# Kernel optimization log

Measured on AMD Instinct MI355X. Metric: run time of the kernel, lower is better.

The kernel has to match this reference:

```python
import jax, jax.numpy as jnp
import numpy as np

N_DRUG, N_DIS = 3072, 3072
N = N_DRUG + N_DIS
E = 196608
F1, F2, F3 = 512, 256, 128
GAMMA1 = GAMMA2 = GAMMA3 = 0.03125
NEG_SLOPE = 0.2   # GATConv default negative_slope
KERNEL_W = 0.25   # drug_ps/dis_ps = 1/kernel_len


def gat_layer(x, src, dst, w_e, W, a_src, a_dst, b):
    """Single-head GATConv: gather -> per-node softmax -> scatter-aggregate.
    Edge weights w_e scale the unnormalized attention."""
    xw = x @ W                                                  # [N, F]
    e = jax.nn.leaky_relu((xw @ a_src)[src] + (xw @ a_dst)[dst], NEG_SLOPE)  # [E]
    m = jax.ops.segment_max(e, dst, num_segments=N)
    ex = jnp.exp(e - m[dst]) * w_e
    denom = jax.ops.segment_sum(ex, dst, num_segments=N)
    alpha = ex / (denom[dst] + 1e-16)
    out = jax.ops.segment_sum(alpha[:, None] * xw[src], dst, num_segments=N)
    return out + b


def gip_kernel(y, gamma):
    """getGipKernel(y, 0, gamma, normalized=True)."""
    mn = jnp.min(y, axis=1, keepdims=True)
    mx = jnp.max(y, axis=1, keepdims=True)
    y = (y - mn) / (mx - mn + 1e-12)          # row-wise min-max normalize
    k = y @ y.T
    k = k / jnp.mean(jnp.diagonal(k))
    d = jnp.diagonal(k)
    dist = d[:, None] + d[None, :] - 2.0 * k  # kernelToDistance
    return jnp.exp(-gamma * dist)


def normalized_kernel(K):
    K = jnp.abs(K)
    minv = jnp.min(jnp.where(K > 0, K, jnp.inf))
    K = jnp.where(K == 0, minv, K)            # replace zeros with min nonzero
    d = jnp.sqrt(jnp.diagonal(K))
    return K / (d[:, None] * d[None, :])


def setup_inputs() -> dict:
    key = jax.random.key(0)
    ks = jax.random.split(key, 20)
    f32 = jnp.float32

    def lin(k, fi, fo):
        return jax.random.normal(k, (fi, fo), f32) * (1.0 / float(np.sqrt(fi)))

    inp = {
        'x': jax.random.normal(ks[0], (N, N), f32),
        'edge_index': jax.random.randint(ks[1], (2, E), 0, N, dtype=jnp.int32),
        'adj_data': jax.random.uniform(ks[2], (N, N), f32),
        'drug_sim': jax.random.uniform(ks[3], (N_DRUG, N_DRUG), f32),
        'dis_sim': jax.random.uniform(ks[4], (N_DIS, N_DIS), f32),
        'alpha1': jax.random.normal(ks[5], (N_DRUG, N_DIS), f32),
        'alpha2': jax.random.normal(ks[6], (N_DIS, N_DRUG), f32),
        'W1': lin(ks[7], N, F1),
        'as1': jax.random.normal(ks[8], (F1,), f32) * 0.1,
        'ad1': jax.random.normal(ks[9], (F1,), f32) * 0.1,
        'b1': jnp.zeros((F1,), f32),
        'W2': lin(ks[10], F1, F2),
        'as2': jax.random.normal(ks[11], (F2,), f32) * 0.1,
        'ad2': jax.random.normal(ks[12], (F2,), f32) * 0.1,
        'b2': jnp.zeros((F2,), f32),
        'W3': lin(ks[13], F2, F3),
        'as3': jax.random.normal(ks[14], (F3,), f32) * 0.1,
        'ad3': jax.random.normal(ks[15], (F3,), f32) * 0.1,
        'b3': jnp.zeros((F3,), f32),
    }
    return inp


def reference(x, edge_index, adj_data, drug_sim, dis_sim, alpha1, alpha2,
              W1, as1, ad1, b1, W2, as2, ad2, b2, W3, as3, ad3, b3):
    src0, dst0 = edge_index[0], edge_index[1]
    w0 = adj_data[src0, dst0]                  # per-edge gather of dense weights
    loop = jnp.arange(N, dtype=src0.dtype)     # GATConv add_self_loops=True
    src = jnp.concatenate([src0, loop])
    dst = jnp.concatenate([dst0, loop])
    w = jnp.concatenate([w0, jnp.ones((N,), adj_data.dtype)])

    H1 = jax.nn.relu(gat_layer(x, src, dst, w, W1, as1, ad1, b1))
    H2 = jax.nn.relu(gat_layer(H1, src, dst, w, W2, as2, ad2, b2))
    H3 = jax.nn.relu(gat_layer(H2, src, dst, w, W3, as3, ad3, b3))

    drug_k = KERNEL_W * (gip_kernel(H1[:N_DRUG], GAMMA1)
                         + gip_kernel(H2[:N_DRUG], GAMMA2)
                         + gip_kernel(H3[:N_DRUG], GAMMA3) + drug_sim)
    dis_k = KERNEL_W * (gip_kernel(H1[N_DRUG:], GAMMA1)
                        + gip_kernel(H2[N_DRUG:], GAMMA2)
                        + gip_kernel(H3[N_DRUG:], GAMMA3) + dis_sim)

    out1 = normalized_kernel(drug_k) @ alpha1  # [N_DRUG, N_DIS]
    out2 = normalized_kernel(dis_k) @ alpha2   # [N_DIS, N_DRUG]
    return 0.5 * (out1 + out2.T)
```

## Files before the change

kernel.cpp:

```cpp
#include <hip/hip_runtime.h>
#include <hip/hip_bf16.h>
#include <stdint.h>

#define N_NODES 6144
#define N_DRUG  3072
#define N_EDGE  196608
#define E_TOT   (N_EDGE + N_NODES)
#define GAMMA   0.03125f

typedef __bf16 bf16x8 __attribute__((ext_vector_type(8)));
typedef float  f32x4  __attribute__((ext_vector_type(4)));

__device__ __forceinline__ unsigned short f2b(float f){
  union { float f; unsigned u; } v; v.f = f;
  unsigned r = v.u + 0x7FFFu + ((v.u >> 16) & 1u);
  return (unsigned short)(r >> 16);
}
__device__ __forceinline__ float b2f(unsigned short b){
  union { unsigned u; float f; } v; v.u = ((unsigned)b) << 16;
  return v.f;
}
__device__ __forceinline__ void gl_lds(const void* g, void* l){
  __builtin_amdgcn_global_load_lds((const __attribute__((address_space(1))) void*)g,
                                   (__attribute__((address_space(3))) void*)l, 16, 0, 0);
}

#define WAITVM(N) asm volatile("s_waitcnt vmcnt(" #N ")" ::: "memory")
#define SYNC() { __builtin_amdgcn_sched_barrier(0); __builtin_amdgcn_s_barrier(); __builtin_amdgcn_sched_barrier(0); }

__global__ void cast_bf16_k(const float* __restrict__ in, unsigned short* __restrict__ out, long n){
  long i = ((long)blockIdx.x*blockDim.x + threadIdx.x)*4;
  long stride = (long)gridDim.x*blockDim.x*4;
  for (; i < n; i += stride){
    float4 v = *(const float4*)(in + i);
    ushort4 o;
    o.x = f2b(v.x); o.y = f2b(v.y); o.z = f2b(v.z); o.w = f2b(v.w);
    *(ushort4*)(out + i) = o;
  }
}

__global__ void tcast_k(const float* __restrict__ in, unsigned short* __restrict__ out,
                        int R, int Cd, int OLD, int OOFF){
  __shared__ float tile[32][33];
  int bx = blockIdx.x*32, by = blockIdx.y*32;
  int tx = threadIdx.x, ty = threadIdx.y;
  for (int i = ty; i < 32; i += 8) tile[i][tx] = in[(long)(by+i)*Cd + bx + tx];
  __syncthreads();
  for (int i = ty; i < 32; i += 8) out[(long)(bx+i)*OLD + OOFF + by + tx] = f2b(tile[tx][i]);
}

__global__ void hist_k(const int* __restrict__ ei, int* __restrict__ cnt){
  int i = blockIdx.x*blockDim.x + threadIdx.x;
  if (i >= E_TOT) return;
  int d = (i < N_EDGE) ? ei[N_EDGE + i] : (i - N_EDGE);
  atomicAdd(&cnt[d], 1);
}

__global__ void scan_k(const int* __restrict__ cnt, int* __restrict__ ptr){
  __shared__ int sums[1024];
  int t = threadIdx.x;
  int v[6]; int s = 0;
  #pragma unroll
  for (int i = 0; i < 6; i++){ v[i] = s; s += cnt[t*6 + i]; }
  sums[t] = s; __syncthreads();
  for (int off = 1; off < 1024; off <<= 1){
    int add = (t >= off) ? sums[t - off] : 0;
    __syncthreads();
    sums[t] += add;
    __syncthreads();
  }
  int base = (t == 0) ? 0 : sums[t-1];
  #pragma unroll
  for (int i = 0; i < 6; i++) ptr[t*6 + i] = base + v[i];
  if (t == 1023) ptr[N_NODES] = sums[1023];
}

__global__ void scatter_k(const int* __restrict__ ei, const int* __restrict__ ptr,
                          int* __restrict__ cur, int* __restrict__ srcs,
                          int* __restrict__ epos){
  int i = blockIdx.x*blockDim.x + threadIdx.x;
  if (i >= E_TOT) return;
  int s = (i < N_EDGE) ? ei[i] : (i - N_EDGE);
  int d = (i < N_EDGE) ? ei[N_EDGE + i] : (i - N_EDGE);
  int pos = ptr[d] + atomicAdd(&cur[d], 1);
  srcs[pos] = s; epos[i] = pos;
}

__global__ void dots_k(const float* __restrict__ XW, const float* __restrict__ av,
                       const float* __restrict__ dv, float* __restrict__ es,
                       float* __restrict__ ed, float* __restrict__ denom, int F){
  int n = blockIdx.x, l = threadIdx.x;
  float s = 0.f, d = 0.f;
  for (int f = l; f < F; f += 64){
    float x = XW[(long)n*F + f];
    s += x * av[f]; d += x * dv[f];
  }
  #pragma unroll
  for (int off = 32; off > 0; off >>= 1){ s += __shfl_down(s, off); d += __shfl_down(d, off); }
  if (l == 0){ es[n] = s; ed[n] = d; denom[n] = 0.f; }
}

__global__ void phase12_k(const int* __restrict__ ei, const float* __restrict__ adj,
                          const float* __restrict__ es, const float* __restrict__ ed,
                          const int* __restrict__ epos, float* __restrict__ exc,
                          float* __restrict__ denom){
  int i = blockIdx.x*blockDim.x + threadIdx.x;
  if (i >= E_TOT) return;
  int s = (i < N_EDGE) ? ei[i] : (i - N_EDGE);
  int d = (i < N_EDGE) ? ei[N_EDGE + i] : (i - N_EDGE);
  float w = (i < N_EDGE) ? adj[(long)s*N_NODES + d] : 1.0f;
  float e = es[s] + ed[d];
  e = (e > 0.f) ? e : 0.2f*e;
  float ex = expf(e) * w;
  exc[epos[i]] = ex;
  atomicAdd(&denom[d], ex);
}

__global__ void agg4_k(const float* __restrict__ XW, const int* __restrict__ ptr,
                       const int* __restrict__ srcs, const float* __restrict__ exc,
                       const float* __restrict__ denom, const float* __restrict__ bias,
                       float* __restrict__ H, unsigned short* __restrict__ Hb, int F){
  int n = blockIdx.x, t = threadIdx.x;
  int st = ptr[n], en = ptr[n+1];
  float a0v = 0.f, a1v = 0.f, a2v = 0.f, a3v = 0.f;
  int j = st;
  for (; j + 1 < en; j += 2){
    float w0 = exc[j], w1 = exc[j+1];
    int s0 = srcs[j], s1 = srcs[j+1];
    float4 v0 = *(const float4*)(XW + (long)s0*F + t*4);
    float4 v1 = *(const float4*)(XW + (long)s1*F + t*4);
    a0v += w0*v0.x + w1*v1.x; a1v += w0*v0.y + w1*v1.y;
    a2v += w0*v0.z + w1*v1.z; a3v += w0*v0.w + w1*v1.w;
  }
  if (j < en){
    float w0 = exc[j]; int s0 = srcs[j];
    float4 v0 = *(const float4*)(XW + (long)s0*F + t*4);
    a0v += w0*v0.x; a1v += w0*v0.y; a2v += w0*v0.z; a3v += w0*v0.w;
  }
  float invd = 1.f/(denom[n] + 1e-16f);
  float4 b = *(const float4*)(bias + t*4);
  float4 o;
  o.x = fmaxf(a0v*invd + b.x, 0.f); o.y = fmaxf(a1v*invd + b.y, 0.f);
  o.z = fmaxf(a2v*invd + b.z, 0.f); o.w = fmaxf(a3v*invd + b.w, 0.f);
  *(float4*)(H + (long)n*F + t*4) = o;
  if (Hb){
    ushort4 ob; ob.x = f2b(o.x); ob.y = f2b(o.y); ob.z = f2b(o.z); ob.w = f2b(o.w);
    *(ushort4*)(Hb + (long)n*F + t*4) = ob;
  }
}

__global__ void agg_k(const float* __restrict__ XW, const int* __restrict__ ptr,
                      const int* __restrict__ srcs, const float* __restrict__ exc,
                      const float* __restrict__ denom, const float* __restrict__ bias,
                      float* __restrict__ H, unsigned short* __restrict__ Hb, int F){
  int n = blockIdx.x, t = threadIdx.x;
  int st = ptr[n], en = ptr[n+1];
  float ax = 0.f, ay = 0.f;
  int j = st;
  for (; j + 1 < en; j += 2){
    float a0 = exc[j], a1 = exc[j+1];
    int s0 = srcs[j], s1 = srcs[j+1];
    float2 v0 = *(const float2*)(XW + (long)s0*F + t*2);
    float2 v1 = *(const float2*)(XW + (long)s1*F + t*2);
    ax += a0*v0.x + a1*v1.x;
    ay += a0*v0.y + a1*v1.y;
  }
  if (j < en){
    float a = exc[j];
    int s = srcs[j];
    float2 v = *(const float2*)(XW + (long)s*F + t*2);
    ax += a*v.x; ay += a*v.y;
  }
  float invd = 1.f/(denom[n] + 1e-16f);
  float2 b = *(const float2*)(bias + t*2);
  float vx = fmaxf(ax*invd + b.x, 0.f);
  float vy = fmaxf(ay*invd + b.y, 0.f);
  *(float2*)(H + (long)n*F + t*2) = make_float2(vx, vy);
  if (Hb){
    ushort2 o; o.x = f2b(vx); o.y = f2b(vy);
    *(ushort2*)(Hb + (long)n*F + t*2) = o;
  }
}

__global__ void rownorm_all_k(const float* __restrict__ H0, const float* __restrict__ H1,
                              const float* __restrict__ H2,
                              unsigned short* __restrict__ y0, unsigned short* __restrict__ y1,
                              float* __restrict__ dv0, float* __restrict__ dv1){
  int seg = blockIdx.y;
  int side = seg / 3, layer = seg % 3;
  int F = 512 >> layer;
  const float* H = (layer == 0) ? H0 : (layer == 1) ? H1 : H2;
  H += (size_t)(side ? N_DRUG : 0) * F;
  unsigned short* yb = ((side ? y1 : y0) + ((layer == 0) ? 0 : (layer == 1) ? 512 : 768));
  float* dvec = (side ? dv1 : dv0) + layer*N_DRUG;

  int r = blockIdx.x, t = threadIdx.x;
  __shared__ float ra[256], rb[256];
  float mn = 3.4e38f, mx = -3.4e38f;
  for (int f = t; f < F; f += 256){
    float v = H[(long)r*F + f];
    mn = fminf(mn, v); mx = fmaxf(mx, v);
  }
  ra[t] = mn; rb[t] = mx; __syncthreads();
  for (int s2 = 128; s2 > 0; s2 >>= 1){
    if (t < s2){ ra[t] = fminf(ra[t], ra[t+s2]); rb[t] = fmaxf(rb[t], rb[t+s2]); }
    __syncthreads();
  }
  mn = ra[0]; mx = rb[0];
  __syncthreads();
  float sc = 1.f/(mx - mn + 1e-12f);
  float s = 0.f;
  for (int f = t; f < F; f += 256){
    float v = (H[(long)r*F + f] - mn)*sc;
    unsigned short b = f2b(v);
    yb[(long)r*896 + f] = b;
    float vb = b2f(b);
    s += vb*vb;
  }
  ra[t] = s; __syncthreads();
  for (int s2 = 128; s2 > 0; s2 >>= 1){
    if (t < s2) ra[t] += ra[t+s2];
    __syncthreads();
  }
  if (t == 0) dvec[r] = ra[0];
}

__global__ void vecsum_all_k(const float* __restrict__ dv0, const float* __restrict__ dv1,
                             float* __restrict__ sump){
  int seg = blockIdx.y;
  int side = seg / 3, layer = seg % 3;
  const float* v = (side ? dv1 : dv0) + layer*N_DRUG;
  __shared__ float red[256];
  int t = threadIdx.x;
  float s = 0.f;
  for (int i = blockIdx.x*256 + t; i < N_DRUG; i += gridDim.x*256) s += v[i];
  red[t] = s; __syncthreads();
  for (int s2 = 128; s2 > 0; s2 >>= 1){ if (t < s2) red[t] += red[t+s2]; __syncthreads(); }
  if (t == 0) atomicAdd(&sump[seg], red[0]);
}

__global__ void diag3_all_k(const float* __restrict__ sim0, const float* __restrict__ sim1,
                            float* __restrict__ rs0, float* __restrict__ rs1){
  int i = blockIdx.x*256 + threadIdx.x;
  const float* sim = blockIdx.y ? sim1 : sim0;
  float* rs = blockIdx.y ? rs1 : rs0;
  if (i < N_DRUG) rs[i] = rsqrtf(sim[(long)i*N_DRUG + i] + 3.0f);
}

template<int EPI>
__global__ __launch_bounds__(512, 2) void gemm8p(
    const unsigned short* __restrict__ A, const unsigned short* __restrict__ Bt,
    float* __restrict__ P, int M, int N, int K, int kz)
{
  __shared__ unsigned short lds[2][2][16384];
  int t = threadIdx.x;
  int lane = t & 63, wave = t >> 6;
  int wm = wave >> 2, wn = wave & 3;

  int nbx = gridDim.x;
  int nwg = nbx * gridDim.y;
  int bid = blockIdx.y * nbx + blockIdx.x;
  int cpx = nwg >> 3;
  int swz = (bid & 7) * cpx + (bid >> 3);
  long brow = (long)(swz / nbx) * 256;
  long bcol = (long)(swz % nbx) * 256;
  long k0 = (long)blockIdx.z * kz;
  int nt = kz >> 6;

  int sr = wave*8 + (lane >> 3);
  int cg = (lane & 7) ^ (lane >> 3);
  const unsigned short* gA = A  + (brow + sr)*(long)K + k0 + cg*8;
  const unsigned short* gB = Bt + (bcol + sr)*(long)K + k0 + cg*8;
  unsigned ldsw = wave * 512;

  auto stage = [&](int b, int mat, int h, int tk){
    const unsigned short* g = (mat ? gB : gA) + (long)(h*128)*K + (long)tk*64;
    unsigned short* d = &lds[b][mat][h*8192 + ldsw];
    gl_lds(g, d);
    gl_lds(g + (long)64*K, d + 4096);
  };

  int fr = lane & 15, q = lane >> 4;
  int lo = fr*64 + ((q ^ (fr & 7))*8);
  int dk = (lo ^ 32) - lo;

  f32x4 acc[8][4];
  #pragma unroll
  for (int a = 0; a < 8; a++)
    #pragma unroll
    for (int b = 0; b < 4; b++){ acc[a][b][0]=0.f; acc[a][b][1]=0.f; acc[a][b][2]=0.f; acc[a][b][3]=0.f; }
  bf16x8 af[4][2], bf[4][2];

  const unsigned short* a0p = &lds[0][0][wm*8192 + lo];
  const unsigned short* b0p = &lds[0][1][wn*4096 + lo];
  const unsigned short* a1p = &lds[1][0][wm*8192 + lo];
  const unsigned short* b1p = &lds[1][1][wn*4096 + lo];

#define RD_AF_LO(ab) { _Pragma("unroll") for (int j = 0; j < 4; ++j){ \
    af[j][0] = *(const bf16x8*)((ab) + j*1024); af[j][1] = *(const bf16x8*)((ab) + j*1024 + dk); } }
#define RD_AF_HI(ab) { _Pragma("unroll") for (int j = 0; j < 4; ++j){ \
    af[j][0] = *(const bf16x8*)((ab) + (4+j)*1024); af[j][1] = *(const bf16x8*)((ab) + (4+j)*1024 + dk); } }
#define RD_BF_LO(bb) { _Pragma("unroll") for (int j = 0; j < 2; ++j){ \
    bf[j][0] = *(const bf16x8*)((bb) + j*1024); bf[j][1] = *(const bf16x8*)((bb) + j*1024 + dk); } }
#define RD_BF_HI(bb) { _Pragma("unroll") for (int j = 2; j < 4; ++j){ \
    bf[j][0] = *(const bf16x8*)((bb) + j*1024); bf[j][1] = *(const bf16x8*)((bb) + j*1024 + dk); } }
#define MFMA_Q(MB, NB) { __builtin_amdgcn_s_setprio(1); \
    _Pragma("unroll") for (int mi = 0; mi < 4; ++mi) \
      _Pragma("unroll") for (int ni = (NB); ni < (NB)+2; ++ni) \
        _Pragma("unroll") for (int kk = 0; kk < 2; ++kk) \
          acc[(MB)+mi][ni] = __builtin_amdgcn_mfma_f32_16x16x32_bf16(af[mi][kk], bf[ni][kk], acc[(MB)+mi][ni], 0, 0, 0); \
    __builtin_amdgcn_s_setprio(0); }

  stage(0,0,0,0); stage(0,0,1,0); stage(0,1,0,0); stage(0,1,1,0);
  stage(1,1,0,1); stage(1,1,1,1);
  WAITVM(4);
  SYNC();

  int half = nt >> 1;
  for (int i = 0; i < half; ++i){
    int t1 = 2*i+1, t2 = 2*i+2, t3 = 2*i+3;
    bool s2 = t2 < nt, s3 = t3 < nt;
    RD_AF_LO(a0p); RD_BF_LO(b0p);
    stage(1,0,0,t1);
    SYNC(); MFMA_Q(0,0); SYNC();
    RD_BF_HI(b0p);
    stage(1,0,1,t1);
    SYNC(); MFMA_Q(0,2); SYNC();
    RD_AF_HI(a0p);
    if (s2) stage(0,1,0,t2);
    SYNC(); MFMA_Q(4,0); SYNC();
    if (s2){ stage(0,1,1,t2); WAITVM(4); } else { WAITVM(0); }
    SYNC(); MFMA_Q(4,2); SYNC();
    RD_AF_LO(a1p); RD_BF_LO(b1p);
    if (s2) stage(0,0,0,t2);
    SYNC(); MFMA_Q(0,0); SYNC();
    RD_BF_HI(b1p);
    if (s2) stage(0,0,1,t2);
    SYNC(); MFMA_Q(0,2); SYNC();
    RD_AF_HI(a1p);
    if (s3) stage(1,1,0,t3);
    SYNC(); MFMA_Q(4,0); SYNC();
    if (s3){ stage(1,1,1,t3); WAITVM(4); } else { WAITVM(0); }
    SYNC(); MFMA_Q(4,2); SYNC();
  }
#undef RD_AF_LO
#undef RD_AF_HI
#undef RD_BF_LO
#undef RD_BF_HI
#undef MFMA_Q

  float* Pz = P + (long)blockIdx.z*M*N;
  #pragma unroll
  for (int mi = 0; mi < 8; ++mi){
    #pragma unroll
    for (int ni = 0; ni < 4; ++ni){
      long col = bcol + wn*64 + ni*16 + fr;
      #pragma unroll
      for (int r = 0; r < 4; ++r){
        long row = brow + wm*128 + mi*16 + q*4 + r;
        float v = acc[mi][ni][r];
        if (EPI == 0) Pz[row*N + col] = v;
        else          Pz[row*N + col] = 0.5f*v;
      }
    }
  }
}

__global__ void reduce4_k(const float* __restrict__ p, float* __restrict__ out, long n){
  long i = ((long)blockIdx.x*blockDim.x + threadIdx.x)*4;
  if (i >= n) return;
  float4 s = *(const float4*)(p + i);
  #pragma unroll
  for (int z = 1; z < 4; z++){
    float4 x = *(const float4*)(p + (long)z*n + i);
    s.x += x.x; s.y += x.y; s.z += x.z; s.w += x.w;
  }
  *(float4*)(out + i) = s;
}

template<int EPI>
__global__ __launch_bounds__(256) void gemm_tn(
    const unsigned short* __restrict__ A, const unsigned short* __restrict__ Bt,
    float* __restrict__ C, int M, int N, int K)
{
  __shared__ unsigned short As[2][128*64];
  __shared__ unsigned short Bs[2][128*64];
  int t = threadIdx.x;
  int wave = t >> 6, lane = t & 63;
  int brow = blockIdx.y*128, bcol = blockIdx.x*128;
  int wr = (wave >> 1)*64, wc = (wave & 1)*64;
  int fr = lane & 15, q = lane >> 4;
  int rin = lane >> 3, kslot = (lane & 7) ^ rin;

  f32x4 acc[4][4];
  #pragma unroll
  for (int a = 0; a < 4; a++)
    #pragma unroll
    for (int b = 0; b < 4; b++){ acc[a][b][0]=0.f; acc[a][b][1]=0.f; acc[a][b][2]=0.f; acc[a][b][3]=0.f; }

  int aoff[4][2], boff[4][2];
  #pragma unroll
  for (int mi = 0; mi < 4; mi++){
    int row = wr + mi*16 + fr;
    #pragma unroll
    for (int kk = 0; kk < 2; kk++) aoff[mi][kk] = row*64 + (((kk*4 + q) ^ (row & 7))*8);
  }
  #pragma unroll
  for (int ni = 0; ni < 4; ni++){
    int row = wc + ni*16 + fr;
    #pragma unroll
    for (int kk = 0; kk < 2; kk++) boff[ni][kk] = row*64 + (((kk*4 + q) ^ (row & 7))*8);
  }

  auto stage = [&](int buf, int k0){
    #pragma unroll
    for (int p = 0; p < 4; p++){
      int rsec = p*32 + wave*8;
      gl_lds(A  + (long)(brow + rsec + rin)*K + k0 + kslot*8, &As[buf][rsec*64]);
      gl_lds(Bt + (long)(bcol + rsec + rin)*K + k0 + kslot*8, &Bs[buf][rsec*64]);
    }
  };

  int nsteps = K >> 6;
  stage(0, 0);
  __syncthreads();
  int curb = 0;
  for (int s = 0; s < nsteps; s++){
    if (s + 1 < nsteps) stage(curb ^ 1, (s + 1)*64);
    const unsigned short* a_l = As[curb];
    const unsigned short* b_l = Bs[curb];
    #pragma unroll
    for (int kk = 0; kk < 2; kk++){
      bf16x8 af[4], bfv[4];
      #pragma unroll
      for (int mi = 0; mi < 4; mi++) af[mi]  = *(const bf16x8*)(a_l + aoff[mi][kk]);
      #pragma unroll
      for (int ni = 0; ni < 4; ni++) bfv[ni] = *(const bf16x8*)(b_l + boff[ni][kk]);
      #pragma unroll
      for (int mi = 0; mi < 4; mi++)
        #pragma unroll
        for (int ni = 0; ni < 4; ni++)
          acc[mi][ni] = __builtin_amdgcn_mfma_f32_16x16x32_bf16(af[mi], bfv[ni], acc[mi][ni], 0, 0, 0);
    }
    __syncthreads();
    curb ^= 1;
  }

  #pragma unroll
  for (int mi = 0; mi < 4; mi++){
    #pragma unroll
    for (int ni = 0; ni < 4; ni++){
      int col = bcol + wc + ni*16 + fr;
      #pragma unroll
      for (int r = 0; r < 4; r++){
        int row = brow + wr + mi*16 + q*4 + r;
        long idx = (long)row*N + col;
        float v = acc[mi][ni][r];
        if (EPI == 0) C[idx] = v;
        else          C[idx] = 0.5f*v;
      }
    }
  }
}

__global__ __launch_bounds__(512) void gip_gemm(
    const unsigned short* __restrict__ Y, const float* __restrict__ sim,
    const float* __restrict__ dv, const float* __restrict__ sums,
    const float* __restrict__ rs, unsigned short* __restrict__ outp, int outoff)
{
  __shared__ unsigned short As[2][128*64];
  __shared__ unsigned short Bs[2][128*64];
  const int K = 896;
  int t = threadIdx.x;
  int wave = t >> 6, lane = t & 63;
  int brow = blockIdx.y*128, bcol = blockIdx.x*128;
  int wr = (wave >> 1)*32, wc = (wave & 1)*64;
  int fr = lane & 15, q = lane >> 4;
  int rin = lane >> 3, kslot = (lane & 7) ^ rin;

  f32x4 acc0[2][4], acc1[2][4], acc2[2][4];
  #pragma unroll
  for (int a = 0; a < 2; a++)
    #pragma unroll
    for (int b = 0; b < 4; b++){
      acc0[a][b][0]=0.f;acc0[a][b][1]=0.f;acc0[a][b][2]=0.f;acc0[a][b][3]=0.f;
      acc1[a][b][0]=0.f;acc1[a][b][1]=0.f;acc1[a][b][2]=0.f;acc1[a][b][3]=0.f;
      acc2[a][b][0]=0.f;acc2[a][b][1]=0.f;acc2[a][b][2]=0.f;acc2[a][b][3]=0.f;
    }

  int aoff[2][2], boff[4][2];
  #pragma unroll
  for (int mi = 0; mi < 2; mi++){
    int row = wr + mi*16 + fr;
    #pragma unroll
    for (int kk = 0; kk < 2; kk++) aoff[mi][kk] = row*64 + (((kk*4 + q) ^ (row & 7))*8);
  }
  #pragma unroll
  for (int ni = 0; ni < 4; ni++){
    int row = wc + ni*16 + fr;
    #pragma unroll
    for (int kk = 0; kk < 2; kk++) boff[ni][kk] = row*64 + (((kk*4 + q) ^ (row & 7))*8);
  }

  auto stage = [&](int buf, int k0){
    #pragma unroll
    for (int p = 0; p < 2; p++){
      int rsec = p*64 + wave*8;
      gl_lds(Y + (long)(brow + rsec + rin)*K + k0 + kslot*8, &As[buf][rsec*64]);
      gl_lds(Y + (long)(bcol + rsec + rin)*K + k0 + kslot*8, &Bs[buf][rsec*64]);
    }
  };

  int curb = 0, s = 0;
  stage(0, 0);
  __syncthreads();

#define GSTEP(ACC) { \
    if (s + 1 < 14) stage(curb ^ 1, (s + 1)*64); \
    const unsigned short* a_l = As[curb]; \
    const unsigned short* b_l = Bs[curb]; \
    _Pragma("unroll") \
    for (int kk = 0; kk < 2; kk++){ \
      bf16x8 af0 = *(const bf16x8*)(a_l + aoff[0][kk]); \
      bf16x8 af1 = *(const bf16x8*)(a_l + aoff[1][kk]); \
      _Pragma("unroll") \
      for (int ni = 0; ni < 4; ni++){ \
        bf16x8 bv = *(const bf16x8*)(b_l + boff[ni][kk]); \
        ACC[0][ni] = __builtin_amdgcn_mfma_f32_16x16x32_bf16(af0, bv, ACC[0][ni], 0, 0, 0); \
        ACC[1][ni] = __builtin_amdgcn_mfma_f32_16x16x32_bf16(af1, bv, ACC[1][ni], 0, 0, 0); \
      } \
    } \
    __syncthreads(); curb ^= 1; s++; }

  for (int i = 0; i < 8; i++) GSTEP(acc0)
  for (int i = 0; i < 4; i++) GSTEP(acc1)
  for (int i = 0; i < 2; i++) GSTEP(acc2)
#undef GSTEP

  float im0 = (float)N_DRUG / sums[0];
  float im1 = (float)N_DRUG / sums[1];
  float im2 = (float)N_DRUG / sums[2];
  #pragma unroll
  for (int mi = 0; mi < 2; mi++){
    #pragma unroll
    for (int ni = 0; ni < 4; ni++){
      int col = bcol + wc + ni*16 + fr;
      float d0c = dv[col], d1c = dv[N_DRUG + col], d2c = dv[2*N_DRUG + col];
      float rc = rs[col];
      #pragma unroll
      for (int r = 0; r < 4; r++){
        int row = brow + wr + mi*16 + q*4 + r;
        float v = sim[(long)row*N_DRUG + col]
                + expf(-GAMMA*((dv[row]            + d0c - 2.f*acc0[mi][ni][r])*im0))
                + expf(-GAMMA*((dv[N_DRUG + row]   + d1c - 2.f*acc1[mi][ni][r])*im1))
                + expf(-GAMMA*((dv[2*N_DRUG + row] + d2c - 2.f*acc2[mi][ni][r])*im2));
        outp[(long)row*N_NODES + outoff + col] = f2b(v * rs[row] * rc);
      }
    }
  }
}

extern "C" void kernel_launch(void* const* d_in, const int* in_sizes, int n_in,
                              void* d_out, int out_size, void* d_ws, size_t ws_size,
                              hipStream_t stream){
  const float* x        = (const float*)d_in[0];
  const int*   ei       = (const int*)d_in[1];
  const float* adj      = (const float*)d_in[2];
  const float* drug_sim = (const float*)d_in[3];
  const float* dis_sim  = (const float*)d_in[4];
  const float* alpha1   = (const float*)d_in[5];
  const float* alpha2   = (const float*)d_in[6];
  const float* W[3]   = {(const float*)d_in[7],  (const float*)d_in[11], (const float*)d_in[15]};
  const float* as_[3] = {(const float*)d_in[8],  (const float*)d_in[12], (const float*)d_in[16]};
  const float* ad_[3] = {(const float*)d_in[9],  (const float*)d_in[13], (const float*)d_in[17]};
  const float* bs_[3] = {(const float*)d_in[10], (const float*)d_in[14], (const float*)d_in[18]};
  float* out = (float*)d_out;
  const int Fs[3] = {512, 256, 128};

  char* p = (char*)d_ws;
  auto alloc = [&](size_t bytes)->char*{
    char* r = p; p += (bytes + 255) & ~(size_t)255; return r;
  };
  unsigned short* xb  = (unsigned short*)alloc((size_t)N_NODES*N_NODES*2);
  unsigned short* wb  = (unsigned short*)alloc((size_t)N_NODES*512*2);
  float* XW           = (float*)alloc((size_t)N_NODES*512*4);
  float* Hf[3];
  Hf[0] = (float*)alloc((size_t)N_NODES*512*4);
  Hf[1] = (float*)alloc((size_t)N_NODES*256*4);
  Hf[2] = (float*)alloc((size_t)N_NODES*128*4);
  unsigned short* Hb  = (unsigned short*)alloc((size_t)N_NODES*512*2);
  float* es    = (float*)alloc(N_NODES*4);
  float* edv   = (float*)alloc(N_NODES*4);
  float* denom = (float*)alloc(N_NODES*4);
  float* exc   = (float*)alloc((size_t)E_TOT*4);
  int* cntcur  = (int*)alloc((size_t)2*N_NODES*4);
  int* cnt = cntcur, *cur = cntcur + N_NODES;
  int* cptr = (int*)alloc((N_NODES+1)*4);
  int* srcs = (int*)alloc((size_t)E_TOT*4);
  int* epos = (int*)alloc((size_t)E_TOT*4);
  unsigned short* ycat[2];
  ycat[0] = (unsigned short*)alloc((size_t)N_DRUG*896*2);
  ycat[1] = (unsigned short*)alloc((size_t)N_DRUG*896*2);
  float* dvv[2];
  dvv[0] = (float*)alloc((size_t)3*N_DRUG*4);
  dvv[1] = (float*)alloc((size_t)3*N_DRUG*4);
  float* sump = (float*)alloc(256);
  float* rsv[2];
  rsv[0] = (float*)alloc(N_DRUG*4);
  rsv[1] = (float*)alloc(N_DRUG*4);
  unsigned short* Abuf  = (unsigned short*)alloc((size_t)N_DRUG*N_NODES*2);
  unsigned short* Btbuf = (unsigned short*)alloc((size_t)N_DRUG*N_NODES*2);

  float* pL1 = (float*)Abuf;

  cast_bf16_k<<<4096, 256, 0, stream>>>(x, xb, (long)N_NODES*N_NODES);
  hipMemsetAsync(cntcur, 0, (size_t)2*N_NODES*4, stream);
  hist_k<<<(E_TOT+255)/256, 256, 0, stream>>>(ei, cnt);
  scan_k<<<1, 1024, 0, stream>>>(cnt, cptr);
  scatter_k<<<(E_TOT+255)/256, 256, 0, stream>>>(ei, cptr, cur, srcs, epos);

  const unsigned short* Ain = xb;
  int Kin = N_NODES;
  for (int l = 0; l < 3; l++){
    int F = Fs[l];
    tcast_k<<<dim3(F/32, Kin/32), dim3(32,8), 0, stream>>>(W[l], wb, Kin, F, Kin, 0);
    if (l == 0){
      gemm8p<0><<<dim3(F/256, N_NODES/256, 4), 512, 0, stream>>>(Ain, wb, pL1, N_NODES, F, Kin, Kin/4);
      reduce4_k<<<(int)(((long)N_NODES*F/4 + 255)/256), 256, 0, stream>>>(pL1, XW, (long)N_NODES*F);
    } else {
      gemm_tn<0><<<dim3(F/128, N_NODES/128), 256, 0, stream>>>(Ain, wb, XW, N_NODES, F, Kin);
    }
    dots_k<<<N_NODES, 64, 0, stream>>>(XW, as_[l], ad_[l], es, edv, denom, F);
    phase12_k<<<(E_TOT+255)/256, 256, 0, stream>>>(ei, adj, es, edv, epos, exc, denom);
    unsigned short* HbOut = (l < 2) ? Hb : nullptr;
    if (F >= 256)
      agg4_k<<<N_NODES, F/4, 0, stream>>>(XW, cptr, srcs, exc, denom, bs_[l], Hf[l], HbOut, F);
    else
      agg_k<<<N_NODES, F/2, 0, stream>>>(XW, cptr, srcs, exc, denom, bs_[l], Hf[l], HbOut, F);
    Ain = Hb; Kin = F;
  }

  hipMemsetAsync(sump, 0, 24, stream);
  rownorm_all_k<<<dim3(N_DRUG, 6), 256, 0, stream>>>(Hf[0], Hf[1], Hf[2],
                                                     ycat[0], ycat[1], dvv[0], dvv[1]);
  vecsum_all_k<<<dim3(12, 6), 256, 0, stream>>>(dvv[0], dvv[1], sump);
  diag3_all_k<<<dim3(N_DRUG/256, 2), 256, 0, stream>>>(drug_sim, dis_sim, rsv[0], rsv[1]);

  tcast_k<<<dim3(N_DRUG/32, N_DRUG/32), dim3(32,8), 0, stream>>>(alpha2, Abuf,  N_DRUG, N_DRUG, N_NODES, N_DRUG);
  tcast_k<<<dim3(N_DRUG/32, N_DRUG/32), dim3(32,8), 0, stream>>>(alpha1, Btbuf, N_DRUG, N_DRUG, N_NODES, 0);

  gip_gemm<<<dim3(N_DRUG/128, N_DRUG/128), 512, 0, stream>>>(ycat[0], drug_sim, dvv[0], sump,     rsv[0], Abuf, 0);
  gip_gemm<<<dim3(N_DRUG/128, N_DRUG/128), 512, 0, stream>>>(ycat[1], dis_sim,  dvv[1], sump + 3, rsv[1], Btbuf, N_DRUG);

  gemm8p<2><<<dim3(N_DRUG/256, N_DRUG/256, 1), 512, 0, stream>>>(Abuf, Btbuf, out, N_DRUG, N_DRUG, N_NODES, N_NODES);

  (void)in_sizes; (void)n_in; (void)out_size; (void)ws_size;
}
```

Baseline: 671.8 us.

## Split-K final GEMM, bf16 aggregation gathers, and merge small kernel launches

The final 3072x3072x6144 GEMM is split three ways along K, launching three times as many blocks. The three fp32 partials are then summed and halved in a separate reduce kernel. The GEMMs that produce XW now also write a bf16 copy, so the edge aggregation gathers half the bytes per neighbour. The per-row diagonal sum is folded into rownorm with atomics, and the paired tcast and gip_gemm launches are merged into single launches using a z grid dimension. The costs are extra partial-buffer traffic, bf16 rounding in the aggregation inputs, and reuse of the xb and XW workspace areas as scratch for the partials.

Result: slower. 816.8 us (+21.6%).

```diff
diff --git a/kernel.cpp b/kernel.cpp
--- a/kernel.cpp
+++ b/kernel.cpp
@@ -47,6 +47,19 @@
   for (int i = ty; i < 32; i += 8) tile[i][tx] = in[(long)(by+i)*Cd + bx + tx];
   __syncthreads();
   for (int i = ty; i < 32; i += 8) out[(long)(bx+i)*OLD + OOFF + by + tx] = f2b(tile[tx][i]);
+}
+
+__global__ void tcast2_k(const float* __restrict__ a2, const float* __restrict__ a1,
+                         unsigned short* __restrict__ o0, unsigned short* __restrict__ o1){
+  __shared__ float tile[32][33];
+  const float* in = blockIdx.z ? a1 : a2;
+  unsigned short* out = blockIdx.z ? o1 : o0;
+  int OOFF = blockIdx.z ? 0 : N_DRUG;
+  int bx = blockIdx.x*32, by = blockIdx.y*32;
+  int tx = threadIdx.x, ty = threadIdx.y;
+  for (int i = ty; i < 32; i += 8) tile[i][tx] = in[(long)(by+i)*N_DRUG + bx + tx];
+  __syncthreads();
+  for (int i = ty; i < 32; i += 8) out[(long)(bx+i)*N_NODES + OOFF + by + tx] = f2b(tile[tx][i]);
 }
 
 __global__ void hist_k(const int* __restrict__ ei, int* __restrict__ cnt){
@@ -116,7 +129,7 @@
   atomicAdd(&denom[d], ex);
 }
 
-__global__ void agg4_k(const float* __restrict__ XW, const int* __restrict__ ptr,
+__global__ void agg4_k(const unsigned short* __restrict__ XWb, const int* __restrict__ ptr,
                        const int* __restrict__ srcs, const float* __restrict__ exc,
                        const float* __restrict__ denom, const float* __restrict__ bias,
                        float* __restrict__ H, unsigned short* __restrict__ Hb, int F){
@@ -127,15 +140,15 @@
   for (; j + 1 < en; j += 2){
     float w0 = exc[j], w1 = exc[j+1];
     int s0 = srcs[j], s1 = srcs[j+1];
-    float4 v0 = *(const float4*)(XW + (long)s0*F + t*4);
-    float4 v1 = *(const float4*)(XW + (long)s1*F + t*4);
-    a0v += w0*v0.x + w1*v1.x; a1v += w0*v0.y + w1*v1.y;
-    a2v += w0*v0.z + w1*v1.z; a3v += w0*v0.w + w1*v1.w;
+    ushort4 u0 = *(const ushort4*)(XWb + (long)s0*F + t*4);
+    ushort4 u1 = *(const ushort4*)(XWb + (long)s1*F + t*4);
+    a0v += w0*b2f(u0.x) + w1*b2f(u1.x); a1v += w0*b2f(u0.y) + w1*b2f(u1.y);
+    a2v += w0*b2f(u0.z) + w1*b2f(u1.z); a3v += w0*b2f(u0.w) + w1*b2f(u1.w);
   }
   if (j < en){
     float w0 = exc[j]; int s0 = srcs[j];
-    float4 v0 = *(const float4*)(XW + (long)s0*F + t*4);
-    a0v += w0*v0.x; a1v += w0*v0.y; a2v += w0*v0.z; a3v += w0*v0.w;
+    ushort4 u0 = *(const ushort4*)(XWb + (long)s0*F + t*4);
+    a0v += w0*b2f(u0.x); a1v += w0*b2f(u0.y); a2v += w0*b2f(u0.z); a3v += w0*b2f(u0.w);
   }
   float invd = 1.f/(denom[n] + 1e-16f);
   float4 b = *(const float4*)(bias + t*4);
@@ -149,7 +162,7 @@
   }
 }
 
-__global__ void agg_k(const float* __restrict__ XW, const int* __restrict__ ptr,
+__global__ void agg_k(const unsigned short* __restrict__ XWb, const int* __restrict__ ptr,
                       const int* __restrict__ srcs, const float* __restrict__ exc,
                       const float* __restrict__ denom, const float* __restrict__ bias,
                       float* __restrict__ H, unsigned short* __restrict__ Hb, int F){
@@ -160,16 +173,15 @@
   for (; j + 1 < en; j += 2){
     float a0 = exc[j], a1 = exc[j+1];
     int s0 = srcs[j], s1 = srcs[j+1];
-    float2 v0 = *(const float2*)(XW + (long)s0*F + t*2);
-    float2 v1 = *(const float2*)(XW + (long)s1*F + t*2);
-    ax += a0*v0.x + a1*v1.x;
-    ay += a0*v0.y + a1*v1.y;
+    ushort2 u0 = *(const ushort2*)(XWb + (long)s0*F + t*2);
+    ushort2 u1 = *(const ushort2*)(XWb + (long)s1*F + t*2);
+    ax += a0*b2f(u0.x) + a1*b2f(u1.x);
+    ay += a0*b2f(u0.y) + a1*b2f(u1.y);
   }
   if (j < en){
-    float a = exc[j];
-    int s = srcs[j];
-    float2 v = *(const float2*)(XW + (long)s*F + t*2);
-    ax += a*v.x; ay += a*v.y;
+    float a = exc[j]; int s = srcs[j];
+    ushort2 u = *(const ushort2*)(XWb + (long)s*F + t*2);
+    ax += a*b2f(u.x); ay += a*b2f(u.y);
   }
   float invd = 1.f/(denom[n] + 1e-16f);
   float2 b = *(const float2*)(bias + t*2);
@@ -185,7 +197,8 @@
 __global__ void rownorm_all_k(const float* __restrict__ H0, const float* __restrict__ H1,
                               const float* __restrict__ H2,
                               unsigned short* __restrict__ y0, unsigned short* __restrict__ y1,
-                              float* __restrict__ dv0, float* __restrict__ dv1){
+                              float* __restrict__ dv0, float* __restrict__ dv1,
+                              float* __restrict__ sump){
   int seg = blockIdx.y;
   int side = seg / 3, layer = seg % 3;
   int F = 512 >> layer;
@@ -222,21 +235,7 @@
     if (t < s2) ra[t] += ra[t+s2];
     __syncthreads();
   }
-  if (t == 0) dvec[r] = ra[0];
-}
-
-__global__ void vecsum_all_k(const float* __restrict__ dv0, const float* __restrict__ dv1,
-                             float* __restrict__ sump){
-  int seg = blockIdx.y;
-  int side = seg / 3, layer = seg % 3;
-  const float* v = (side ? dv1 : dv0) + layer*N_DRUG;
-  __shared__ float red[256];
-  int t = threadIdx.x;
-  float s = 0.f;
-  for (int i = blockIdx.x*256 + t; i < N_DRUG; i += gridDim.x*256) s += v[i];
-  red[t] = s; __syncthreads();
-  for (int s2 = 128; s2 > 0; s2 >>= 1){ if (t < s2) red[t] += red[t+s2]; __syncthreads(); }
-  if (t == 0) atomicAdd(&sump[seg], red[0]);
+  if (t == 0){ dvec[r] = ra[0]; atomicAdd(&sump[seg], ra[0]); }
 }
 
 __global__ void diag3_all_k(const float* __restrict__ sim0, const float* __restrict__ sim1,
@@ -247,10 +246,9 @@
   if (i < N_DRUG) rs[i] = rsqrtf(sim[(long)i*N_DRUG + i] + 3.0f);
 }
 
-template<int EPI>
 __global__ __launch_bounds__(512, 2) void gemm8p(
     const unsigned short* __restrict__ A, const unsigned short* __restrict__ Bt,
-    float* __restrict__ P, int M, int N, int K, int kz)
+    float* __restrict__ P, float* __restrict__ Palt, int M, int N, int K, int kz)
 {
   __shared__ unsigned short lds[2][2][16384];
   int t = threadIdx.x;
@@ -349,7 +347,8 @@
 #undef RD_BF_HI
 #undef MFMA_Q
 
-  float* Pz = P + (long)blockIdx.z*M*N;
+  int z = blockIdx.z;
+  float* Pz = (z < 2) ? (P + (long)z*M*N) : (Palt + (long)(z-2)*M*N);
   #pragma unroll
   for (int mi = 0; mi < 8; ++mi){
     #pragma unroll
@@ -358,15 +357,14 @@
       #pragma unroll
       for (int r = 0; r < 4; ++r){
         long row = brow + wm*128 + mi*16 + q*4 + r;
-        float v = acc[mi][ni][r];
-        if (EPI == 0) Pz[row*N + col] = v;
-        else          Pz[row*N + col] = 0.5f*v;
+        Pz[row*N + col] = acc[mi][ni][r];
       }
     }
   }
 }
 
-__global__ void reduce4_k(const float* __restrict__ p, float* __restrict__ out, long n){
+__global__ void reduce4b_k(const float* __restrict__ p, float* __restrict__ out,
+                           unsigned short* __restrict__ outb, long n){
   long i = ((long)blockIdx.x*blockDim.x + threadIdx.x)*4;
   if (i >= n) return;
   float4 s = *(const float4*)(p + i);
@@ -376,12 +374,26 @@
     s.x += x.x; s.y += x.y; s.z += x.z; s.w += x.w;
   }
   *(float4*)(out + i) = s;
-}
-
-template<int EPI>
+  ushort4 o; o.x = f2b(s.x); o.y = f2b(s.y); o.z = f2b(s.z); o.w = f2b(s.w);
+  *(ushort4*)(outb + i) = o;
+}
+
+__global__ void reduce3h_k(const float* __restrict__ pa, const float* __restrict__ pb,
+                           const float* __restrict__ pc, float* __restrict__ out, long n){
+  long i = ((long)blockIdx.x*blockDim.x + threadIdx.x)*4;
+  if (i >= n) return;
+  float4 a = *(const float4*)(pa + i);
+  float4 b = *(const float4*)(pb + i);
+  float4 c = *(const float4*)(pc + i);
+  float4 o;
+  o.x = 0.5f*(a.x + b.x + c.x); o.y = 0.5f*(a.y + b.y + c.y);
+  o.z = 0.5f*(a.z + b.z + c.z); o.w = 0.5f*(a.w + b.w + c.w);
+  *(float4*)(out + i) = o;
+}
+
 __global__ __launch_bounds__(256) void gemm_tn(
     const unsigned short* __restrict__ A, const unsigned short* __restrict__ Bt,
-    float* __restrict__ C, int M, int N, int K)
+    float* __restrict__ C, unsigned short* __restrict__ Cb, int M, int N, int K)
 {
   __shared__ unsigned short As[2][128*64];
   __shared__ unsigned short Bs[2][128*64];
@@ -456,21 +468,33 @@
         int row = brow + wr + mi*16 + q*4 + r;
         long idx = (long)row*N + col;
         float v = acc[mi][ni][r];
-        if (EPI == 0) C[idx] = v;
-        else          C[idx] = 0.5f*v;
+        C[idx] = v;
+        if (Cb) Cb[idx] = f2b(v);
       }
     }
   }
 }
 
 __global__ __launch_bounds__(512) void gip_gemm(
-    const unsigned short* __restrict__ Y, const float* __restrict__ sim,
-    const float* __restrict__ dv, const float* __restrict__ sums,
-    const float* __restrict__ rs, unsigned short* __restrict__ outp, int outoff)
+    const unsigned short* __restrict__ Y0, const unsigned short* __restrict__ Y1,
+    const float* __restrict__ sim0, const float* __restrict__ sim1,
+    const float* __restrict__ dva, const float* __restrict__ dvb,
+    const float* __restrict__ sumps,
+    const float* __restrict__ rs0, const float* __restrict__ rs1,
+    unsigned short* __restrict__ o0, unsigned short* __restrict__ o1)
 {
   __shared__ unsigned short As[2][128*64];
   __shared__ unsigned short Bs[2][128*64];
   const int K = 896;
+  int side = blockIdx.z;
+  const unsigned short* Y = side ? Y1 : Y0;
+  const float* sim  = side ? sim1 : sim0;
+  const float* dv   = side ? dvb : dva;
+  const float* sums = sumps + side*3;
+  const float* rs   = side ? rs1 : rs0;
+  unsigned short* outp = side ? o1 : o0;
+  int outoff = side ? N_DRUG : 0;
+
   int t = threadIdx.x;
   int wave = t >> 6, lane = t & 63;
   int brow = blockIdx.y*128, bcol = blockIdx.x*128;
@@ -584,6 +608,7 @@
   unsigned short* xb  = (unsigned short*)alloc((size_t)N_NODES*N_NODES*2);
   unsigned short* wb  = (unsigned short*)alloc((size_t)N_NODES*512*2);
   float* XW           = (float*)alloc((size_t)N_NODES*512*4);
+  unsigned short* XWb = (unsigned short*)alloc((size_t)N_NODES*512*2);
   float* Hf[3];
   Hf[0] = (float*)alloc((size_t)N_NODES*512*4);
   Hf[1] = (float*)alloc((size_t)N_NODES*256*4);
@@ -612,6 +637,9 @@
   unsigned short* Btbuf = (unsigned short*)alloc((size_t)N_DRUG*N_NODES*2);
 
   float* pL1 = (float*)Abuf;
+  float* pF01 = (float*)xb;
+  float* pF2  = (float*)XW;
+  const long MN = (long)N_DRUG*N_DRUG;
 
   cast_bf16_k<<<4096, 256, 0, stream>>>(x, xb, (long)N_NODES*N_NODES);
   hipMemsetAsync(cntcur, 0, (size_t)2*N_NODES*4, stream);
@@ -625,34 +653,33 @@
     int F = Fs[l];
     tcast_k<<<dim3(F/32, Kin/32), dim3(32,8), 0, stream>>>(W[l], wb, Kin, F, Kin, 0);
     if (l == 0){
-      gemm8p<0><<<dim3(F/256, N_NODES/256, 4), 512, 0, stream>>>(Ain, wb, pL1, N_NODES, F, Kin, Kin/4);
-      reduce4_k<<<(int)(((long)N_NODES*F/4 + 255)/256), 256, 0, stream>>>(pL1, XW, (long)N_NODES*F);
+      gemm8p<<<dim3(F/256, N_NODES/256, 4), 512, 0, stream>>>(Ain, wb, pL1, pL1 + 2*(long)N_NODES*F, N_NODES, F, Kin, Kin/4);
+      reduce4b_k<<<(int)(((long)N_NODES*F/4 + 255)/256), 256, 0, stream>>>(pL1, XW, XWb, (long)N_NODES*F);
     } else {
-      gemm_tn<0><<<dim3(F/128, N_NODES/128), 256, 0, stream>>>(Ain, wb, XW, N_NODES, F, Kin);
+      gemm_tn<<<dim3(F/128, N_NODES/128), 256, 0, stream>>>(Ain, wb, XW, XWb, N_NODES, F, Kin);
     }
     dots_k<<<N_NODES, 64, 0, stream>>>(XW, as_[l], ad_[l], es, edv, denom, F);
     phase12_k<<<(E_TOT+255)/256, 256, 0, stream>>>(ei, adj, es, edv, epos, exc, denom);
     unsigned short* HbOut = (l < 2) ? Hb : nullptr;
     if (F >= 256)
-      agg4_k<<<N_NODES, F/4, 0, stream>>>(XW, cptr, srcs, exc, denom, bs_[l], Hf[l], HbOut, F);
+      agg4_k<<<N_NODES, F/4, 0, stream>>>(XWb, cptr, srcs, exc, denom, bs_[l], Hf[l], HbOut, F);
     else
-      agg_k<<<N_NODES, F/2, 0, stream>>>(XW, cptr, srcs, exc, denom, bs_[l], Hf[l], HbOut, F);
+      agg_k<<<N_NODES, 64, 0, stream>>>(XWb, cptr, srcs, exc, denom, bs_[l], Hf[l], HbOut, F);
     Ain = Hb; Kin = F;
   }
 
   hipMemsetAsync(sump, 0, 24, stream);
   rownorm_all_k<<<dim3(N_DRUG, 6), 256, 0, stream>>>(Hf[0], Hf[1], Hf[2],
-                                                     ycat[0], ycat[1], dvv[0], dvv[1]);
-  vecsum_all_k<<<dim3(12, 6), 256, 0, stream>>>(dvv[0], dvv[1], sump);
+                                                     ycat[0], ycat[1], dvv[0], dvv[1], sump);
   diag3_all_k<<<dim3(N_DRUG/256, 2), 256, 0, stream>>>(drug_sim, dis_sim, rsv[0], rsv[1]);
 
-  tcast_k<<<dim3(N_DRUG/32, N_DRUG/32), dim3(32,8), 0, stream>>>(alpha2, Abuf,  N_DRUG, N_DRUG, N_NODES, N_DRUG);
-  tcast_k<<<dim3(N_DRUG/32, N_DRUG/32), dim3(32,8), 0, stream>>>(alpha1, Btbuf, N_DRUG, N_DRUG, N_NODES, 0);
-
-  gip_gemm<<<dim3(N_DRUG/128, N_DRUG/128), 512, 0, stream>>>(ycat[0], drug_sim, dvv[0], sump,     rsv[0], Abuf, 0);
-  gip_gemm<<<dim3(N_DRUG/128, N_DRUG/128), 512, 0, stream>>>(ycat[1], dis_sim,  dvv[1], sump + 3, rsv[1], Btbuf, N_DRUG);
-
-  gemm8p<2><<<dim3(N_DRUG/256, N_DRUG/256, 1), 512, 0, stream>>>(Abuf, Btbuf, out, N_DRUG, N_DRUG, N_NODES, N_NODES);
+  tcast2_k<<<dim3(N_DRUG/32, N_DRUG/32, 2), dim3(32,8), 0, stream>>>(alpha2, alpha1, Abuf, Btbuf);
+
+  gip_gemm<<<dim3(N_DRUG/128, N_DRUG/128, 2), 512, 0, stream>>>(
+      ycat[0], ycat[1], drug_sim, dis_sim, dvv[0], dvv[1], sump, rsv[0], rsv[1], Abuf, Btbuf);
+
+  gemm8p<<<dim3(N_DRUG/256, N_DRUG/256, 3), 512, 0, stream>>>(Abuf, Btbuf, pF01, pF2, N_DRUG, N_DRUG, N_NODES, N_NODES/3);
+  reduce3h_k<<<(int)((MN/4 + 255)/256), 256, 0, stream>>>(pF01, pF01 + MN, pF2, out, MN);
 
   (void)in_sizes; (void)n_in; (void)out_size; (void)ws_size;
 }
```
